# Kernel optimization log

Measured on AMD Instinct MI355X. Metric: run time of the kernel, lower is better.

## Reference

```python
import jax, jax.numpy as jnp
import numpy as np

H = 64  # GRU hidden size


def _gru_scan(x_proj, m, U, b_rec):
    # x_proj: [S,B,3H] precomputed input projections (time-major); m: [S,B] bool mask
    B = x_proj.shape[1]
    h0 = jnp.zeros((B, H), x_proj.dtype)

    def step(h, inp):
        xp, mt = inp
        rec = h @ U + b_rec                       # [B,3H] (Keras reset_after=True)
        xz, xr, xh = jnp.split(xp, 3, axis=-1)
        rz, rr, rh = jnp.split(rec, 3, axis=-1)
        z = jax.nn.sigmoid(xz + rz)
        r = jax.nn.sigmoid(xr + rr)
        hh = jnp.tanh(xh + r * rh)
        hn = z * h + (1.0 - z) * hh
        hn = jnp.where(mt[:, None], hn, h)        # masked steps carry state through
        return hn, hn

    hT, hs = jax.lax.scan(step, h0, (x_proj, m))
    return hs, hT  # hs: [S,B,H], hT: [B,H]


def setup_inputs() -> dict:
    key = jax.random.key(0)
    ks = jax.random.split(key, 16)
    V, E = 50000, 25
    B, S, T = 512, 200, 10
    s = 0.05
    f32 = jnp.float32
    inp = {
        "input_batch": jax.random.randint(ks[0], (B, S, T), 0, V),
        "emb_table": jax.random.normal(ks[1], (V, E), f32) * s,
        "W_f": jax.random.normal(ks[2], (E, 3 * H), f32) * s,
        "U_f": jax.random.normal(ks[3], (H, 3 * H), f32) * s,
        "b_f": jnp.zeros((2, 3 * H), f32),
        "W_b": jax.random.normal(ks[4], (E, 3 * H), f32) * s,
        "U_b": jax.random.normal(ks[5], (H, 3 * H), f32) * s,
        "b_b": jnp.zeros((2, 3 * H), f32),
        "W_k": jax.random.normal(ks[6], (2 * H, H), f32) * s,
        "b_k": jnp.zeros((H,), f32),
        "W_q": jax.random.normal(ks[7], (H, H), f32) * s,
        "b_q": jnp.zeros((H,), f32),
        "W_e": jax.random.normal(ks[8], (H, 1), f32) * s,
        "b_e": jnp.zeros((1,), f32),
    }
    return inp


def reference(input_batch, emb_table, W_f, U_f, b_f, W_b, U_b, b_b, W_k, b_k, W_q, b_q, W_e, b_e):
    mask = input_batch != 0                                  # [B,S,T]
    emb = emb_table[input_batch]                             # [B,S,T,E]
    nm = mask.astype(emb.dtype)
    denom = nm.sum(axis=2)                                   # [B,S]
    denom = jnp.where(denom == 0, jnp.ones_like(denom), denom)
    x = (emb * nm[..., None]).sum(axis=2) / denom[..., None] # [B,S,E] masked mean over tags
    step_mask = mask[:, :, 0]                                # [B,S] GRU step mask

    xT = jnp.swapaxes(x, 0, 1)                               # [S,B,E]
    mT = jnp.swapaxes(step_mask, 0, 1)                       # [S,B]

    # forward GRU
    hs_f, hT_f = _gru_scan(xT @ W_f + b_f[0], mT, U_f, b_f[1])
    # backward GRU: reverse time, scan, reverse back
    hs_b, _ = _gru_scan((xT @ W_b + b_b[0])[::-1], mT[::-1], U_b, b_b[1])
    hs_b = hs_b[::-1]

    out = jnp.swapaxes(jnp.concatenate([hs_f, hs_b], axis=-1), 0, 1)  # [B,S,2H]

    # Bahdanau attention; query = forward final state
    keys = out @ W_k + b_k                                   # [B,S,H]
    queries = hT_f @ W_q + b_q                               # [B,H]
    e = jnp.tanh(keys + queries[:, None, :]) @ W_e + b_e     # [B,S,1]
    e = e + (1.0 - step_mask.astype(e.dtype))[..., None] * -1e9
    w = jax.nn.softmax(e, axis=1)                            # [B,S,1]
    context = (w * out).sum(axis=1)                          # [B,2H]
    return context
```

## Files before the change

### kernel.cpp

```cpp
#include <hip/hip_runtime.h>
#include <math.h>

#define BATCH 512
#define SEQ   200
#define TOK   10
#define EMB   25
#define XPAD  28
#define HID   64
#define G3    192
#define ATILE 8

__device__ __forceinline__ float fast_sigmoid(float t) {
    float e = __expf(-t);
    return __builtin_amdgcn_rcpf(1.f + e);
}
__device__ __forceinline__ float fast_tanh(float t) {
    float e2 = __expf(2.f * t);
    return 1.f - 2.f * __builtin_amdgcn_rcpf(e2 + 1.f);
}

#define LDS_BARRIER() do {                                   \
    asm volatile("s_waitcnt lgkmcnt(0)" ::: "memory");       \
    __builtin_amdgcn_s_barrier();                            \
    asm volatile("" ::: "memory");                           \
} while (0)

__global__ __launch_bounds__(256) void emb_mean_kernel(
    const int* __restrict__ ids_g, const float* __restrict__ emb,
    float* __restrict__ x, float* __restrict__ mask)
{
    int grp  = blockIdx.x * 8 + (threadIdx.x >> 5);
    int lane = threadIdx.x & 31;
    if (grp >= BATCH * SEQ) return;
    const int* ids = ids_g + (size_t)grp * TOK;
    float acc = 0.f;
    int cnt = 0;
    #pragma unroll
    for (int t = 0; t < TOK; t++) {
        int id = ids[t];
        if (id != 0) {
            cnt++;
            if (lane < EMB) acc += emb[(size_t)id * EMB + lane];
        }
    }
    if (lane < EMB)
        x[(size_t)grp * EMB + lane] = cnt ? acc / (float)cnt : 0.f;
    if (lane == 0)
        mask[grp] = (ids[0] != 0) ? 1.f : 0.f;
}


#define U_LIST(M) \
  M(0)  M(1)  M(2)  M(3)  M(4)  M(5)  M(6)  M(7)  \
  M(8)  M(9)  M(10) M(11) M(12) M(13) M(14) M(15) \
  M(16) M(17) M(18) M(19) M(20) M(21) M(22) M(23) \
  M(24) M(25) M(26) M(27) M(28) M(29) M(30) M(31) \
  M(32) M(33) M(34) M(35) M(36) M(37) M(38) M(39) \
  M(40) M(41) M(42) M(43) M(44) M(45) M(46) M(47) \
  M(48) M(49) M(50) M(51) M(52) M(53) M(54) M(55) \
  M(56) M(57) M(58) M(59) M(60) M(61) M(62) M(63)

#define W_LIST(M) \
  M(0)  M(1)  M(2)  M(3)  M(4)  M(5)  M(6)  M(7)  \
  M(8)  M(9)  M(10) M(11) M(12) M(13) M(14) M(15) \
  M(16) M(17) M(18) M(19) M(20) M(21) M(22) M(23) M(24)

#define DECL_U(i) const float u##i = U[(i) * G3 + col];
#define DECL_W(i) const float w##i = W[(i) * G3 + col];

#define REC4(q, i0, i1, i2, i3) {                 \
    const float4 hv = hs4[q];                     \
    a0 = fmaf(hv.x, u##i0, a0);                   \
    a1 = fmaf(hv.y, u##i1, a1);                   \
    a2 = fmaf(hv.z, u##i2, a2);                   \
    a3 = fmaf(hv.w, u##i3, a3); }

#define X4(q, i0, i1, i2, i3) {                   \
    const float4 xv = xr4[q];                     \
    p0 = fmaf(xv.x, w##i0, p0);                   \
    p1 = fmaf(xv.y, w##i1, p1);                   \
    p2 = fmaf(xv.z, w##i2, p2);                   \
    p3 = fmaf(xv.w, w##i3, p3); }

#define XPROJ(P, XR) do {                                         \
    const float4* xr4 = (const float4*)(XR);                      \
    float p0 = bx, p1 = 0.f, p2 = 0.f, p3 = 0.f;                  \
    X4(0, 0, 1, 2, 3)   X4(1, 4, 5, 6, 7)   X4(2, 8, 9, 10, 11)  \
    X4(3, 12, 13, 14, 15) X4(4, 16, 17, 18, 19) X4(5, 20, 21, 22, 23) \
    p0 = fmaf((XR)[24], w24, p0);                                 \
    P = (p0 + p1) + (p2 + p3);                                    \
} while (0)

__global__ __launch_bounds__(192, 3) void gru_kernel(
    const float* __restrict__ xg, const float* __restrict__ maskg,
    const float* __restrict__ W_f, const float* __restrict__ U_f, const float* __restrict__ b_f,
    const float* __restrict__ W_b, const float* __restrict__ U_b, const float* __restrict__ b_b,
    float* __restrict__ outg, float* __restrict__ hT)
{
    const int bidx = blockIdx.x;
    const int dir  = bidx >> 9;
    const int b    = bidx & 511;
    const int tid  = threadIdx.x;
    const int w    = tid >> 6;
    const int j    = tid & 63;

    const float* W    = dir ? W_b : W_f;
    const float* U    = dir ? U_b : U_f;
    const float* bias = dir ? b_b : b_f;

    const int col = w * HID + j;

    U_LIST(DECL_U)
    W_LIST(DECL_W)
    const float bx = bias[col];
    const float br = bias[G3 + col];

    __shared__ __align__(16) float xs[SEQ * XPAD];
    __shared__ float ms[SEQ];
    __shared__ __align__(16) float hs[HID];
    __shared__ float zs[HID];
    __shared__ float rs[HID];

    {
        for (int i = tid; i < SEQ * EMB; i += 192) {
            int s = i / EMB;
            int e = i - s * EMB;
            xs[s * XPAD + e] = xg[(size_t)b * (SEQ * EMB) + i];
        }
        for (int i = tid; i < SEQ; i += 192) ms[i] = maskg[(size_t)b * SEQ + i];
        if (tid < HID) hs[tid] = 0.f;
    }
    __syncthreads();

    const float4* hs4 = (const float4*)hs;
    float h = 0.f;
    float* obase = outg + (size_t)b * SEQ * (2 * HID) + dir * HID + j;

    float p;
    {
        const int s0 = dir ? (SEQ - 1) : 0;
        XPROJ(p, xs + s0 * XPAD);
    }

    for (int step = 0; step < SEQ; step++) {
        const int s = dir ? (SEQ - 1 - step) : step;

        float a0 = br, a1 = 0.f, a2 = 0.f, a3 = 0.f;
        REC4(0,  0,  1,  2,  3)   REC4(1,  4,  5,  6,  7)
        REC4(2,  8,  9, 10, 11)   REC4(3, 12, 13, 14, 15)
        REC4(4, 16, 17, 18, 19)   REC4(5, 20, 21, 22, 23)
        REC4(6, 24, 25, 26, 27)   REC4(7, 28, 29, 30, 31)
        REC4(8, 32, 33, 34, 35)   REC4(9, 36, 37, 38, 39)
        REC4(10, 40, 41, 42, 43)  REC4(11, 44, 45, 46, 47)
        REC4(12, 48, 49, 50, 51)  REC4(13, 52, 53, 54, 55)
        REC4(14, 56, 57, 58, 59)  REC4(15, 60, 61, 62, 63)
        const float a = (a0 + a1) + (a2 + a3);

        if (w == 0)      zs[j] = fast_sigmoid(p + a);
        else if (w == 1) rs[j] = fast_sigmoid(p + a);

        LDS_BARRIER();

        if (w == 2) {
            float r  = rs[j];
            float z  = zs[j];
            float hh = fast_tanh(p + r * a);
            float hn = z * h + (1.f - z) * hh;
            hn = (ms[s] != 0.f) ? hn : h;
            h = hn;
            hs[j] = hn;
            obase[(size_t)s * (2 * HID)] = hn;
        }

        {
            const int sn  = dir ? (SEQ - 2 - step) : (step + 1);
            const int snc = (step + 1 < SEQ) ? sn : s;
            XPROJ(p, xs + snc * XPAD);
        }

        LDS_BARRIER();
    }
    if (w == 2 && dir == 0) hT[(size_t)b * HID + j] = h;
}


#define WK_LIST(M) \
  M(0)  M(1)  M(2)  M(3)  M(4)  M(5)  M(6)  M(7)  \
  M(8)  M(9)  M(10) M(11) M(12) M(13) M(14) M(15) \
  M(16) M(17) M(18) M(19) M(20) M(21) M(22) M(23) \
  M(24) M(25) M(26) M(27) M(28) M(29) M(30) M(31)

#define DECL_WK(t) const float wk##t = W_k[(size_t)(32 * wave + (t)) * HID + lane];

#define KF4(q, t0, t1, t2, t3) {                  \
    const float4 ov = o4[q];                      \
    acc0 = fmaf(ov.x, wk##t0, acc0);              \
    acc1 = fmaf(ov.y, wk##t1, acc1);              \
    acc0 = fmaf(ov.z, wk##t2, acc0);              \
    acc1 = fmaf(ov.w, wk##t3, acc1); }

__global__ __launch_bounds__(256) void attn_kernel(
    const float* __restrict__ outg, const float* __restrict__ maskg,
    const float* __restrict__ hT,
    const float* __restrict__ W_k, const float* __restrict__ b_k,
    const float* __restrict__ W_q, const float* __restrict__ b_q,
    const float* __restrict__ W_e, const float* __restrict__ b_e,
    float* __restrict__ ctx)
{
    const int b    = blockIdx.x;
    const int tid  = threadIdx.x;
    const int wave = tid >> 6;
    const int lane = tid & 63;

    __shared__ float qs[HID];
    __shared__ float es[SEQ];
    __shared__ __align__(16) float kp[ATILE][4][HID];
    __shared__ __align__(16) float psum[4][2 * HID];

    WK_LIST(DECL_WK)

    const float bkj = b_k[lane];
    const float wej = W_e[lane];
    const float be  = b_e[0];

    if (tid < HID) {
        float q = b_q[tid];
        const float* hrow = hT + (size_t)b * HID;
        #pragma unroll 8
        for (int i = 0; i < HID; i++) q = fmaf(hrow[i], W_q[i * HID + tid], q);
        qs[tid] = q;
    }
    __syncthreads();
    const float qj = qs[lane];

    for (int s0 = 0; s0 < SEQ; s0 += ATILE) {
        #pragma unroll 2
        for (int t = 0; t < ATILE; t++) {
            const int s = s0 + t;
            const float4* o4 = (const float4*)(outg +
                ((size_t)b * SEQ + s) * (2 * HID) + 32 * wave);
            float acc0 = 0.f, acc1 = 0.f;
            KF4(0,  0,  1,  2,  3)  KF4(1,  4,  5,  6,  7)
            KF4(2,  8,  9, 10, 11)  KF4(3, 12, 13, 14, 15)
            KF4(4, 16, 17, 18, 19)  KF4(5, 20, 21, 22, 23)
            KF4(6, 24, 25, 26, 27)  KF4(7, 28, 29, 30, 31)
            kp[t][wave][lane] = acc0 + acc1;
        }
        __syncthreads();
        #pragma unroll
        for (int t = wave; t < ATILE; t += 4) {
            const int s = s0 + t;
            float k = (kp[t][0][lane] + kp[t][1][lane]) +
                      (kp[t][2][lane] + kp[t][3][lane]);
            float v = tanhf(k + bkj + qj) * wej;
            #pragma unroll
            for (int off = 32; off > 0; off >>= 1) v += __shfl_xor(v, off);
            if (lane == 0) {
                float pen = (maskg[(size_t)b * SEQ + s] != 0.f) ? 0.f : -1e9f;
                es[s] = v + be + pen;
            }
        }
        __syncthreads();
    }

    if (tid < 64) {
        float mx = -1e30f;
        for (int s2 = tid; s2 < SEQ; s2 += 64) mx = fmaxf(mx, es[s2]);
        #pragma unroll
        for (int off = 32; off > 0; off >>= 1) mx = fmaxf(mx, __shfl_xor(mx, off));
        float sum = 0.f;
        for (int s2 = tid; s2 < SEQ; s2 += 64) {
            float w = expf(es[s2] - mx);
            es[s2] = w;
            sum += w;
        }
        #pragma unroll
        for (int off = 32; off > 0; off >>= 1) sum += __shfl_xor(sum, off);
        float inv = 1.f / sum;
        for (int s2 = tid; s2 < SEQ; s2 += 64) es[s2] *= inv;
    }
    __syncthreads();

    {
        float a0 = 0.f, a1 = 0.f;
        #pragma unroll 2
        for (int s2 = wave; s2 < SEQ; s2 += 4) {
            const float2 v = *(const float2*)(outg +
                ((size_t)b * SEQ + s2) * (2 * HID) + lane * 2);
            const float wsc = es[s2];
            a0 = fmaf(wsc, v.x, a0);
            a1 = fmaf(wsc, v.y, a1);
        }
        psum[wave][2 * lane]     = a0;
        psum[wave][2 * lane + 1] = a1;
    }
    __syncthreads();
    if (tid < 2 * HID) {
        ctx[(size_t)b * (2 * HID) + tid] =
            (psum[0][tid] + psum[1][tid]) + (psum[2][tid] + psum[3][tid]);
    }
}

extern "C" void kernel_launch(void* const* d_in, const int* in_sizes, int n_in,
                              void* d_out, int out_size, void* d_ws, size_t ws_size,
                              hipStream_t stream) {
    const int*   ids = (const int*)  d_in[0];
    const float* emb = (const float*)d_in[1];
    const float* W_f = (const float*)d_in[2];
    const float* U_f = (const float*)d_in[3];
    const float* b_f = (const float*)d_in[4];
    const float* W_b = (const float*)d_in[5];
    const float* U_b = (const float*)d_in[6];
    const float* b_b = (const float*)d_in[7];
    const float* W_k = (const float*)d_in[8];
    const float* b_k = (const float*)d_in[9];
    const float* W_q = (const float*)d_in[10];
    const float* b_q = (const float*)d_in[11];
    const float* W_e = (const float*)d_in[12];
    const float* b_e = (const float*)d_in[13];

    float* ws   = (float*)d_ws;
    float* x    = ws;
    float* mask = ws + 2560000;
    float* out  = ws + 2662400;
    float* hT   = ws + 15769600;

    emb_mean_kernel<<<(BATCH * SEQ) / 8, 256, 0, stream>>>(ids, emb, x, mask);
    gru_kernel<<<1024, 192, 0, stream>>>(x, mask, W_f, U_f, b_f,
                                         W_b, U_b, b_b, out, hT);
    attn_kernel<<<BATCH, 256, 0, stream>>>(out, mask, hT, W_k, b_k,
                                           W_q, b_q, W_e, b_e, (float*)d_out);
}
```

Measured before the change: 430.4 us.

## Process two batch rows per GRU block and stream transposed U from global

```diff
diff --git a/kernel.cpp b/kernel.cpp
--- a/kernel.cpp
+++ b/kernel.cpp
@@ -9,6 +9,8 @@
 #define HID   64
 #define G3    192
 #define ATILE 8
+#define EMB_BLOCKS ((BATCH * SEQ) / 8)
+#define UT2_BLOCKS 96
 
 __device__ __forceinline__ float fast_sigmoid(float t) {
     float e = __expf(-t);
@@ -27,11 +29,22 @@
 
 __global__ __launch_bounds__(256) void emb_mean_kernel(
     const int* __restrict__ ids_g, const float* __restrict__ emb,
-    float* __restrict__ x, float* __restrict__ mask)
+    const float* __restrict__ U_f, const float* __restrict__ U_b,
+    float* __restrict__ x, float* __restrict__ mask, float* __restrict__ ut2)
 {
+    if (blockIdx.x >= EMB_BLOCKS) {
+        const int eb = blockIdx.x - EMB_BLOCKS;
+        const int dir = eb / 48;
+        const int g   = (eb % 48) / 16;
+        const int c   = eb % 16;
+        const int t   = threadIdx.x;
+        const int jj  = t >> 2, q = t & 3;
+        const float* U = dir ? U_b : U_f;
+        ut2[(size_t)eb * 256 + t] = U[(size_t)(4 * c + q) * G3 + g * HID + jj];
+        return;
+    }
     int grp  = blockIdx.x * 8 + (threadIdx.x >> 5);
     int lane = threadIdx.x & 31;
-    if (grp >= BATCH * SEQ) return;
     const int* ids = ids_g + (size_t)grp * TOK;
     float acc = 0.f;
     int cnt = 0;
@@ -50,30 +63,12 @@
 }
 
 
-#define U_LIST(M) \
-  M(0)  M(1)  M(2)  M(3)  M(4)  M(5)  M(6)  M(7)  \
-  M(8)  M(9)  M(10) M(11) M(12) M(13) M(14) M(15) \
-  M(16) M(17) M(18) M(19) M(20) M(21) M(22) M(23) \
-  M(24) M(25) M(26) M(27) M(28) M(29) M(30) M(31) \
-  M(32) M(33) M(34) M(35) M(36) M(37) M(38) M(39) \
-  M(40) M(41) M(42) M(43) M(44) M(45) M(46) M(47) \
-  M(48) M(49) M(50) M(51) M(52) M(53) M(54) M(55) \
-  M(56) M(57) M(58) M(59) M(60) M(61) M(62) M(63)
-
 #define W_LIST(M) \
   M(0)  M(1)  M(2)  M(3)  M(4)  M(5)  M(6)  M(7)  \
   M(8)  M(9)  M(10) M(11) M(12) M(13) M(14) M(15) \
   M(16) M(17) M(18) M(19) M(20) M(21) M(22) M(23) M(24)
 
-#define DECL_U(i) const float u##i = U[(i) * G3 + col];
 #define DECL_W(i) const float w##i = W[(i) * G3 + col];
-
-#define REC4(q, i0, i1, i2, i3) {                 \
-    const float4 hv = hs4[q];                     \
-    a0 = fmaf(hv.x, u##i0, a0);                   \
-    a1 = fmaf(hv.y, u##i1, a1);                   \
-    a2 = fmaf(hv.z, u##i2, a2);                   \
-    a3 = fmaf(hv.w, u##i3, a3); }
 
 #define X4(q, i0, i1, i2, i3) {                   \
     const float4 xv = xr4[q];                     \
@@ -91,96 +86,125 @@
     P = (p0 + p1) + (p2 + p3);                                    \
 } while (0)
 
-__global__ __launch_bounds__(192, 3) void gru_kernel(
+__global__ __launch_bounds__(192, 2) void gru_kernel(
     const float* __restrict__ xg, const float* __restrict__ maskg,
-    const float* __restrict__ W_f, const float* __restrict__ U_f, const float* __restrict__ b_f,
-    const float* __restrict__ W_b, const float* __restrict__ U_b, const float* __restrict__ b_b,
+    const float* __restrict__ W_f, const float* __restrict__ b_f,
+    const float* __restrict__ W_b, const float* __restrict__ b_b,
+    const float* __restrict__ ut2,
     float* __restrict__ outg, float* __restrict__ hT)
 {
-    const int bidx = blockIdx.x;
-    const int dir  = bidx >> 9;
-    const int b    = bidx & 511;
+    const int bid  = blockIdx.x;
+    const int dir  = bid >> 8;
+    const int pair = bid & 255;
+    const int b0   = pair * 2;
+    const int b1   = b0 + 1;
     const int tid  = threadIdx.x;
-    const int w    = tid >> 6;
+    const int g    = tid >> 6;
     const int j    = tid & 63;
 
     const float* W    = dir ? W_b : W_f;
-    const float* U    = dir ? U_b : U_f;
     const float* bias = dir ? b_b : b_f;
-
-    const int col = w * HID + j;
-
-    U_LIST(DECL_U)
+    const int col = g * HID + j;
+
     W_LIST(DECL_W)
     const float bx = bias[col];
     const float br = bias[G3 + col];
 
-    __shared__ __align__(16) float xs[SEQ * XPAD];
-    __shared__ float ms[SEQ];
-    __shared__ __align__(16) float hs[HID];
-    __shared__ float zs[HID];
-    __shared__ float rs[HID];
-
-    {
-        for (int i = tid; i < SEQ * EMB; i += 192) {
-            int s = i / EMB;
-            int e = i - s * EMB;
-            xs[s * XPAD + e] = xg[(size_t)b * (SEQ * EMB) + i];
-        }
-        for (int i = tid; i < SEQ; i += 192) ms[i] = maskg[(size_t)b * SEQ + i];
-        if (tid < HID) hs[tid] = 0.f;
-    }
+    __shared__ __align__(16) float xs[2][SEQ * XPAD];
+    __shared__ float ms[2][SEQ];
+    __shared__ __align__(16) float hs[2][HID];
+    __shared__ float zs[2][HID];
+    __shared__ float rs[2][HID];
+
+    for (int i = tid; i < SEQ * EMB; i += 192) {
+        int s_ = i / EMB;
+        int e_ = i - s_ * EMB;
+        xs[0][s_ * XPAD + e_] = xg[(size_t)b0 * (SEQ * EMB) + i];
+        xs[1][s_ * XPAD + e_] = xg[(size_t)b1 * (SEQ * EMB) + i];
+    }
+    for (int i = tid; i < SEQ; i += 192) {
+        ms[0][i] = maskg[(size_t)b0 * SEQ + i];
+        ms[1][i] = maskg[(size_t)b1 * SEQ + i];
+    }
+    if (tid < HID) { hs[0][tid] = 0.f; hs[1][tid] = 0.f; }
     __syncthreads();
 
-    const float4* hs4 = (const float4*)hs;
-    float h = 0.f;
-    float* obase = outg + (size_t)b * SEQ * (2 * HID) + dir * HID + j;
-
-    float p;
+    const float* ub = ut2 + (size_t)(dir * 3 + g) * 16 * 256 + j * 4;
+
+    float h0 = 0.f, h1 = 0.f;
+    float* ob0 = outg + (size_t)b0 * SEQ * (2 * HID) + dir * HID + j;
+    float* ob1 = outg + (size_t)b1 * SEQ * (2 * HID) + dir * HID + j;
+
+    float p0x, p1x;
     {
         const int s0 = dir ? (SEQ - 1) : 0;
-        XPROJ(p, xs + s0 * XPAD);
+        XPROJ(p0x, &xs[0][s0 * XPAD]);
+        XPROJ(p1x, &xs[1][s0 * XPAD]);
     }
 
     for (int step = 0; step < SEQ; step++) {
         const int s = dir ? (SEQ - 1 - step) : step;
 
+        const float4* h40 = (const float4*)hs[0];
+        const float4* h41 = (const float4*)hs[1];
+        const float* up = ub;
+        asm volatile("" : "+v"(up));
+
         float a0 = br, a1 = 0.f, a2 = 0.f, a3 = 0.f;
-        REC4(0,  0,  1,  2,  3)   REC4(1,  4,  5,  6,  7)
-        REC4(2,  8,  9, 10, 11)   REC4(3, 12, 13, 14, 15)
-        REC4(4, 16, 17, 18, 19)   REC4(5, 20, 21, 22, 23)
-        REC4(6, 24, 25, 26, 27)   REC4(7, 28, 29, 30, 31)
-        REC4(8, 32, 33, 34, 35)   REC4(9, 36, 37, 38, 39)
-        REC4(10, 40, 41, 42, 43)  REC4(11, 44, 45, 46, 47)
-        REC4(12, 48, 49, 50, 51)  REC4(13, 52, 53, 54, 55)
-        REC4(14, 56, 57, 58, 59)  REC4(15, 60, 61, 62, 63)
+        float c0 = br, c1 = 0.f, c2 = 0.f, c3 = 0.f;
+        #pragma unroll
+        for (int c = 0; c < 16; c++) {
+            const float4 u  = *(const float4*)(up + c * 256);
+            const float4 v0 = h40[c];
+            const float4 v1 = h41[c];
+            a0 = fmaf(v0.x, u.x, a0);  a1 = fmaf(v0.y, u.y, a1);
+            a2 = fmaf(v0.z, u.z, a2);  a3 = fmaf(v0.w, u.w, a3);
+            c0 = fmaf(v1.x, u.x, c0);  c1 = fmaf(v1.y, u.y, c1);
+            c2 = fmaf(v1.z, u.z, c2);  c3 = fmaf(v1.w, u.w, c3);
+        }
         const float a = (a0 + a1) + (a2 + a3);
-
-        if (w == 0)      zs[j] = fast_sigmoid(p + a);
-        else if (w == 1) rs[j] = fast_sigmoid(p + a);
+        const float c = (c0 + c1) + (c2 + c3);
+
+        if (g == 0) {
+            zs[0][j] = fast_sigmoid(p0x + a);
+            zs[1][j] = fast_sigmoid(p1x + c);
+        } else if (g == 1) {
+            rs[0][j] = fast_sigmoid(p0x + a);
+            rs[1][j] = fast_sigmoid(p1x + c);
+        }
 
         LDS_BARRIER();
 
-        if (w == 2) {
-            float r  = rs[j];
-            float z  = zs[j];
-            float hh = fast_tanh(p + r * a);
-            float hn = z * h + (1.f - z) * hh;
-            hn = (ms[s] != 0.f) ? hn : h;
-            h = hn;
-            hs[j] = hn;
-            obase[(size_t)s * (2 * HID)] = hn;
+        if (g == 2) {
+            float r0 = rs[0][j], z0 = zs[0][j];
+            float hh0 = fast_tanh(p0x + r0 * a);
+            float hn0 = z0 * h0 + (1.f - z0) * hh0;
+            hn0 = (ms[0][s] != 0.f) ? hn0 : h0;
+            h0 = hn0;
+            hs[0][j] = hn0;
+            ob0[(size_t)s * (2 * HID)] = hn0;
+            float r1 = rs[1][j], z1 = zs[1][j];
+            float hh1 = fast_tanh(p1x + r1 * c);
+            float hn1 = z1 * h1 + (1.f - z1) * hh1;
+            hn1 = (ms[1][s] != 0.f) ? hn1 : h1;
+            h1 = hn1;
+            hs[1][j] = hn1;
+            ob1[(size_t)s * (2 * HID)] = hn1;
         }
 
         {
             const int sn  = dir ? (SEQ - 2 - step) : (step + 1);
             const int snc = (step + 1 < SEQ) ? sn : s;
-            XPROJ(p, xs + snc * XPAD);
+            XPROJ(p0x, &xs[0][snc * XPAD]);
+            XPROJ(p1x, &xs[1][snc * XPAD]);
         }
 
         LDS_BARRIER();
     }
-    if (w == 2 && dir == 0) hT[(size_t)b * HID + j] = h;
+    if (g == 2 && dir == 0) {
+        hT[(size_t)b0 * HID + j] = h0;
+        hT[(size_t)b1 * HID + j] = h1;
+    }
 }
 
 
@@ -324,10 +348,12 @@
     float* mask = ws + 2560000;
     float* out  = ws + 2662400;
     float* hT   = ws + 15769600;
-
-    emb_mean_kernel<<<(BATCH * SEQ) / 8, 256, 0, stream>>>(ids, emb, x, mask);
-    gru_kernel<<<1024, 192, 0, stream>>>(x, mask, W_f, U_f, b_f,
-                                         W_b, U_b, b_b, out, hT);
+    float* ut2  = ws + 15802368;
+
+    emb_mean_kernel<<<EMB_BLOCKS + UT2_BLOCKS, 256, 0, stream>>>(
+        ids, emb, U_f, U_b, x, mask, ut2);
+    gru_kernel<<<512, 192, 0, stream>>>(x, mask, W_f, b_f, W_b, b_b, ut2,
+                                        out, hT);
     attn_kernel<<<BATCH, 256, 0, stream>>>(out, mask, hT, W_k, b_k,
                                            W_q, b_q, W_e, b_e, (float*)d_out);
 }
```

Result: slower. 743.5 us (+72.8%).
